# Kernel optimization log

Hardware: AMD Instinct MI355X
Metric: run time of the kernel (lower is better)

Reference implementation:

```python
import jax, jax.numpy as jnp
from jax import lax
import numpy as np

SEQ, BATCH, IN, H = 512, 256, 180, 8


def _lstm_layer(x, w_ih, w_hh, b_ih, b_hh):
    # x: [S, B, I]; PyTorch gate order: i, f, g, o stacked along 4H
    S, B, _ = x.shape
    Hh = w_hh.shape[1]
    # input contribution for all timesteps at once (one big GEMM)
    xg = jnp.einsum('sbi,gi->sbg', x, w_ih) + b_ih + b_hh  # [S, B, 4H]

    def step(carry, xt):
        h, c = carry
        g = xt + h @ w_hh.T  # [B, 4H]
        i, f, gg, o = jnp.split(g, 4, axis=-1)
        i = jax.nn.sigmoid(i)
        f = jax.nn.sigmoid(f)
        gg = jnp.tanh(gg)
        o = jax.nn.sigmoid(o)
        c = f * c + i * gg
        h = o * jnp.tanh(c)
        return (h, c), h

    init = (jnp.zeros((B, Hh), x.dtype), jnp.zeros((B, Hh), x.dtype))
    _, ys = lax.scan(step, init, xg)
    return ys  # [S, B, H]


def setup_inputs() -> dict:
    key = jax.random.key(0)
    ks = jax.random.split(key, 11)
    s = 1.0 / np.sqrt(H)  # PyTorch LSTM init scale
    return {
        'x': jax.random.normal(ks[0], (SEQ, BATCH, IN), jnp.float32),
        'w_ih0': jax.random.uniform(ks[1], (4 * H, IN), jnp.float32, -s, s),
        'w_hh0': jax.random.uniform(ks[2], (4 * H, H), jnp.float32, -s, s),
        'b_ih0': jax.random.uniform(ks[3], (4 * H,), jnp.float32, -s, s),
        'b_hh0': jax.random.uniform(ks[4], (4 * H,), jnp.float32, -s, s),
        'w_ih1': jax.random.uniform(ks[5], (4 * H, H), jnp.float32, -s, s),
        'w_hh1': jax.random.uniform(ks[6], (4 * H, H), jnp.float32, -s, s),
        'b_ih1': jax.random.uniform(ks[7], (4 * H,), jnp.float32, -s, s),
        'b_hh1': jax.random.uniform(ks[8], (4 * H,), jnp.float32, -s, s),
        'w_reg': jax.random.uniform(ks[9], (2, H), jnp.float32, -s, s),
        'b_reg': jax.random.uniform(ks[10], (2,), jnp.float32, -s, s),
    }


def reference(x, w_ih0, w_hh0, b_ih0, b_hh0, w_ih1, w_hh1, b_ih1, b_hh1, w_reg, b_reg):
    h1 = _lstm_layer(x, w_ih0, w_hh0, b_ih0, b_hh0)   # [S, B, H]
    h2 = _lstm_layer(h1, w_ih1, w_hh1, b_ih1, b_hh1)  # [S, B, H]
    S, B, Hh = h2.shape
    flat = h2.reshape(S * B, Hh)
    return flat @ w_reg.T + b_reg  # [S*B, 2]
```

## Files before the change

kernel.cpp:

```cpp
#include <hip/hip_runtime.h>

#define S_  512
#define B_  256
#define NIN 180

typedef float v2 __attribute__((ext_vector_type(2)));

#define SSIG  -1.4426950408889634f
#define STANH -2.8853900817779268f

#define QP_X1 0xB1
#define QP_X2 0x4E
#define QP_X3 0x1B
#define ROR4  0x124
#define ROR8  0x128

template<int CTRL>
__device__ __forceinline__ float dppf(float x) {
    return __uint_as_float((unsigned)__builtin_amdgcn_update_dpp(
        0, (int)__float_as_uint(x), CTRL, 0xF, 0xF, true));
}

#define ROTS8(h, r) do { \
    r[0] = (h); \
    r[1] = dppf<QP_X1>(h); \
    r[2] = dppf<QP_X2>(h); \
    r[3] = dppf<QP_X3>(h); \
    r[4] = dppf<ROR4>(h); \
    r[5] = dppf<QP_X1>(r[4]); \
    r[6] = dppf<QP_X2>(r[4]); \
    r[7] = dppf<QP_X3>(r[4]); \
} while (0)

__global__ __launch_bounds__(256) void xg_gemm(
    const float* __restrict__ x, const float* __restrict__ w,
    const float* __restrict__ bi, const float* __restrict__ bh,
    float* __restrict__ xg2)
{
    __shared__ float wt[NIN][32];
    __shared__ float bias[32];
    const int tid = threadIdx.x;
    for (int idx = tid; idx < NIN * 32; idx += 256) {
        int g = idx / NIN, i = idx - g * NIN;
        float sc = ((g >> 3) == 2) ? STANH : SSIG;
        wt[i][g] = sc * w[idx];
    }
    if (tid < 32) {
        float sc = ((tid >> 3) == 2) ? STANH : SSIG;
        bias[tid] = sc * (bi[tid] + bh[tid]);
    }
    __syncthreads();

    const int rg = tid >> 3;
    const int gq = tid & 7;
    const int s  = blockIdx.x >> 1;
    const int b0 = (blockIdx.x & 1) * 128 + rg * 4;
    const float* xr = x + ((size_t)s * B_ + b0) * NIN;

    float4 acc[4];
    #pragma unroll
    for (int r = 0; r < 4; ++r) acc[r] = float4{0.f, 0.f, 0.f, 0.f};

    float4 rv[2][4];
    #pragma unroll
    for (int r = 0; r < 4; ++r) {
        rv[0][r] = *(const float4*)(xr + (size_t)r * NIN + 0);
        rv[1][r] = *(const float4*)(xr + (size_t)r * NIN + 4);
    }

    #pragma unroll
    for (int ii = 0; ii < 45; ++ii) {
        const int sl = ii & 1;
        float4 xa[4];
        #pragma unroll
        for (int r = 0; r < 4; ++r) xa[r] = rv[sl][r];
        if (ii < 43) {
            #pragma unroll
            for (int r = 0; r < 4; ++r)
                rv[sl][r] = *(const float4*)(xr + (size_t)r * NIN + 4 * (ii + 2));
        }
        #pragma unroll
        for (int e = 0; e < 4; ++e) {
            float4 wv = *(const float4*)&wt[4 * ii + e][gq * 4];
            #pragma unroll
            for (int r = 0; r < 4; ++r) {
                float xe = (e == 0) ? xa[r].x : (e == 1) ? xa[r].y
                         : (e == 2) ? xa[r].z : xa[r].w;
                acc[r].x = __builtin_fmaf(xe, wv.x, acc[r].x);
                acc[r].y = __builtin_fmaf(xe, wv.y, acc[r].y);
                acc[r].z = __builtin_fmaf(xe, wv.z, acc[r].z);
                acc[r].w = __builtin_fmaf(xe, wv.w, acc[r].w);
            }
        }
    }

    float4 bv = *(const float4*)&bias[gq * 4];
    const int g0 = 4 * gq, q = g0 >> 3, j0 = g0 & 7, cls = q >> 1, qb = q & 1;
    #pragma unroll
    for (int r = 0; r < 4; ++r) {
        int b = b0 + r;
        size_t base = (((size_t)s * 64 + (b >> 2)) * 64
                      + (b & 3) * 16 + qb * 8 + j0) * 2 + cls;
        xg2[base + 0] = acc[r].x + bv.x;
        xg2[base + 2] = acc[r].y + bv.y;
        xg2[base + 4] = acc[r].z + bv.z;
        xg2[base + 6] = acc[r].w + bv.w;
    }
}

__global__ __launch_bounds__(128, 1) void lstm_scan(
    const float* __restrict__ xg,
    const float* __restrict__ w_hh0,
    const float* __restrict__ w_ih1, const float* __restrict__ w_hh1,
    const float* __restrict__ b_ih1, const float* __restrict__ b_hh1,
    const float* __restrict__ w_reg, const float* __restrict__ b_reg,
    float* __restrict__ out)
{
    __shared__ float a1buf[2][128];

    const int lt = threadIdx.x & 63;
    const int j  = lt & 7;
    const int b3 = (lt >> 3) & 1;
    const int cc = lt >> 4;
    const bool b3z = (b3 == 0);
    const int bid = blockIdx.x;

    const int gA = b3 * 8 + j;
    const int gB = (2 + b3) * 8 + j;
    const float sB_ = b3z ? STANH : SSIG;
    const float aB  = b3z ? 2.0f : 1.0f;
    const float bB  = b3z ? -1.0f : 0.0f;

    auto COMBINE2 = [&](float tA, float tB, float& c, float& h) {
        float m  = tA * tB;
        float mr = dppf<ROR8>(m);
        float fa = dppf<ROR8>(tA);
        float ob = dppf<ROR8>(tB);
        float ig = b3z ? m  : mr;
        float f  = b3z ? fa : tA;
        float o  = b3z ? ob : tB;
        c = __builtin_fmaf(f, c, ig);
        float th = __builtin_fmaf(2.0f, __builtin_amdgcn_rcpf(
            1.0f + __builtin_amdgcn_exp2f(STANH * c)), -1.0f);
        h = o * th;
    };

    if (threadIdx.x < 64) {
        v2 w0p[8], wi1p[8];
        #pragma unroll
        for (int m = 0; m < 8; ++m) {
            int k = j ^ m;
            w0p[m]  = v2{SSIG * w_hh0[gA * 8 + k], sB_ * w_hh0[gB * 8 + k]};
            wi1p[m] = v2{SSIG * w_ih1[gA * 8 + k], sB_ * w_ih1[gB * 8 + k]};
        }
        const v2 b1p = v2{SSIG * (b_ih1[gA] + b_hh1[gA]),
                          sB_  * (b_ih1[gB] + b_hh1[gB])};

        float h0p = 0.f, c0v = 0.f;
        const float* xrow = xg + (size_t)bid * 128;
        v2 xq[8];
        #pragma unroll
        for (int k2 = 0; k2 < 8; ++k2) {
            xq[k2] = *(const v2*)(xrow + lt * 2);
            xrow += 8192;
        }

        auto ASTEP = [&](v2& xr, int slot, bool pref) {
            v2 xc = xr;
            if (pref) { xr = *(const v2*)(xrow + lt * 2); xrow += 8192; }
            float r0[8];
            ROTS8(h0p, r0);
            v2 a0 = xc, a1p = b1p;
            #pragma unroll
            for (int m = 0; m < 8; ++m) {
                v2 rm = v2{r0[m], r0[m]};
                a0  = __builtin_elementwise_fma(w0p[m], rm, a0);
                a1p = __builtin_elementwise_fma(wi1p[m], rm, a1p);
            }
            *(v2*)&a1buf[slot][lt * 2] = a1p;
            float eA = __builtin_amdgcn_exp2f(a0.x);
            float eB = __builtin_amdgcn_exp2f(a0.y);
            float tA = __builtin_amdgcn_rcpf(1.0f + eA);
            float tB = __builtin_fmaf(aB, __builtin_amdgcn_rcpf(1.0f + eB), bB);
            COMBINE2(tA, tB, c0v, h0p);
            __syncthreads();
        };

        #pragma unroll
        for (int k2 = 0; k2 < 8; ++k2) ASTEP(xq[k2], k2 & 1, true);
        for (int tb = 8; tb < 504; tb += 8) {
            #pragma unroll
            for (int k2 = 0; k2 < 8; ++k2) ASTEP(xq[k2], k2 & 1, true);
        }
        #pragma unroll
        for (int k2 = 0; k2 < 8; ++k2) ASTEP(xq[k2], k2 & 1, false);

        {
            float r0[8];
            ROTS8(h0p, r0);
            v2 a1p = b1p;
            #pragma unroll
            for (int m = 0; m < 8; ++m) {
                v2 rm = v2{r0[m], r0[m]};
                a1p = __builtin_elementwise_fma(wi1p[m], rm, a1p);
            }
            *(v2*)&a1buf[0][lt * 2] = a1p;
            __syncthreads();
        }
    } else {
        v2 wh1p[8];
        float wrl[8];
        #pragma unroll
        for (int m = 0; m < 8; ++m) {
            int k = j ^ m;
            wh1p[m] = v2{SSIG * w_hh1[gA * 8 + k], sB_ * w_hh1[gB * 8 + k]};
            wrl[m]  = w_reg[b3 * 8 + k];
        }
        const float br  = b_reg[b3];
        const bool isl  = (j == 0);
        const int  ooff = (bid * 4 + cc) * 2 + b3;

        float h1p = 0.f, c1v = 0.f;

        auto BSTEP = [&](int slot, bool dostore, int yrow) {
            v2 a1 = *(const v2*)&a1buf[slot][lt * 2];
            float r1[8];
            ROTS8(h1p, r1);
            #pragma unroll
            for (int m = 0; m < 8; ++m) {
                v2 rm = v2{r1[m], r1[m]};
                a1 = __builtin_elementwise_fma(wh1p[m], rm, a1);
            }
            float p = br;
            #pragma unroll
            for (int m = 0; m < 8; ++m) p = __builtin_fmaf(wrl[m], r1[m], p);
            float eA = __builtin_amdgcn_exp2f(a1.x);
            float eB = __builtin_amdgcn_exp2f(a1.y);
            float tA = __builtin_amdgcn_rcpf(1.0f + eA);
            float tB = __builtin_fmaf(aB, __builtin_amdgcn_rcpf(1.0f + eB), bB);
            if (dostore && isl) out[(size_t)yrow * 512 + ooff] = p;
            COMBINE2(tA, tB, c1v, h1p);
        };

        __syncthreads();
        __syncthreads();
        for (int u = 2; u < 512; ++u) {
            BSTEP((u - 1) & 1, u >= 3, u - 3);
            __syncthreads();
        }
        BSTEP(1, true, 509);
        __syncthreads();
        BSTEP(0, true, 510);
        {
            float r1[8];
            ROTS8(h1p, r1);
            float p = br;
            #pragma unroll
            for (int m = 0; m < 8; ++m) p = __builtin_fmaf(wrl[m], r1[m], p);
            if (isl) out[(size_t)511 * 512 + ooff] = p;
        }
    }
}

extern "C" void kernel_launch(void* const* d_in, const int* in_sizes, int n_in,
                              void* d_out, int out_size, void* d_ws, size_t ws_size,
                              hipStream_t stream) {
    (void)in_sizes; (void)n_in; (void)out_size; (void)ws_size;
    const float* x     = (const float*)d_in[0];
    const float* w_ih0 = (const float*)d_in[1];
    const float* w_hh0 = (const float*)d_in[2];
    const float* b_ih0 = (const float*)d_in[3];
    const float* b_hh0 = (const float*)d_in[4];
    const float* w_ih1 = (const float*)d_in[5];
    const float* w_hh1 = (const float*)d_in[6];
    const float* b_ih1 = (const float*)d_in[7];
    const float* b_hh1 = (const float*)d_in[8];
    const float* w_reg = (const float*)d_in[9];
    const float* b_reg = (const float*)d_in[10];
    float* out = (float*)d_out;
    float* xg2 = (float*)d_ws;

    xg_gemm<<<1024, 256, 0, stream>>>(x, w_ih0, b_ih0, b_hh0, xg2);
    lstm_scan<<<64, 128, 0, stream>>>(xg2, w_hh0, w_ih1, w_hh1, b_ih1, b_hh1,
                                      w_reg, b_reg, out);
}
```

Measured before the change: 136.3 us.

## Batch layer handoff through 16-slot ring and retile xg GEMM to 8 rows per thread

The scan kernel's layer-0 wave now writes layer-1 input contributions into a 16-slot shared ring and synchronises once every four timesteps instead of every step. The layer-1 wave consumes the ring with matching barriers and runs the output projection only when it is needed. The input GEMM is retiled so each thread computes 8 batch rows with packed v2 FMAs and a 3-deep prefetch, using a permuted weight column order so it can write float4 stores. The fewer barriers should shorten the serial scan, at the cost of more shared memory, more registers and more complex indexing.

```diff
diff --git a/kernel.cpp b/kernel.cpp
--- a/kernel.cpp
+++ b/kernel.cpp
@@ -41,70 +41,84 @@
     __shared__ float bias[32];
     const int tid = threadIdx.x;
     for (int idx = tid; idx < NIN * 32; idx += 256) {
-        int g = idx / NIN, i = idx - g * NIN;
+        int c = idx / NIN, i = idx - c * NIN;
+        int t = c >> 2, e = c & 3;
+        int g = (t >> 2) * 8 + (t & 3) * 2 + (e >> 1) + ((e & 1) << 4);
         float sc = ((g >> 3) == 2) ? STANH : SSIG;
-        wt[i][g] = sc * w[idx];
+        wt[i][c] = sc * w[g * NIN + i];
     }
     if (tid < 32) {
-        float sc = ((tid >> 3) == 2) ? STANH : SSIG;
-        bias[tid] = sc * (bi[tid] + bh[tid]);
+        int c = tid, t = c >> 2, e = c & 3;
+        int g = (t >> 2) * 8 + (t & 3) * 2 + (e >> 1) + ((e & 1) << 4);
+        float sc = ((g >> 3) == 2) ? STANH : SSIG;
+        bias[c] = sc * (bi[g] + bh[g]);
     }
     __syncthreads();
 
     const int rg = tid >> 3;
-    const int gq = tid & 7;
-    const int s  = blockIdx.x >> 1;
-    const int b0 = (blockIdx.x & 1) * 128 + rg * 4;
+    const int t8 = tid & 7;
+    const int s  = blockIdx.x;
+    const int b0 = rg * 8;
     const float* xr = x + ((size_t)s * B_ + b0) * NIN;
 
-    float4 acc[4];
+    v2 acc[8][2];
     #pragma unroll
-    for (int r = 0; r < 4; ++r) acc[r] = float4{0.f, 0.f, 0.f, 0.f};
-
-    float4 rv[2][4];
+    for (int r = 0; r < 8; ++r) { acc[r][0] = v2{0.f, 0.f}; acc[r][1] = v2{0.f, 0.f}; }
+
+    float4 xb[3][8];
     #pragma unroll
-    for (int r = 0; r < 4; ++r) {
-        rv[0][r] = *(const float4*)(xr + (size_t)r * NIN + 0);
-        rv[1][r] = *(const float4*)(xr + (size_t)r * NIN + 4);
-    }
-
+    for (int d = 0; d < 3; ++d)
+        #pragma unroll
+        for (int r = 0; r < 8; ++r)
+            xb[d][r] = *(const float4*)(xr + (size_t)r * NIN + 4 * d);
+
+    auto GSTEP = [&](int ii, int d, bool pref) {
+        float4 xn[8];
+        if (pref) {
+            #pragma unroll
+            for (int r = 0; r < 8; ++r)
+                xn[r] = *(const float4*)(xr + (size_t)r * NIN + 4 * (ii + 3));
+        }
+        #pragma unroll
+        for (int e = 0; e < 4; ++e) {
+            float4 wv = *(const float4*)&wt[4 * ii + e][t8 * 4];
+            v2 wlo = v2{wv.x, wv.y}, whi = v2{wv.z, wv.w};
+            #pragma unroll
+            for (int r = 0; r < 8; ++r) {
+                float xe = (e == 0) ? xb[d][r].x : (e == 1) ? xb[d][r].y
+                         : (e == 2) ? xb[d][r].z : xb[d][r].w;
+                v2 xv = v2{xe, xe};
+                acc[r][0] = __builtin_elementwise_fma(wlo, xv, acc[r][0]);
+                acc[r][1] = __builtin_elementwise_fma(whi, xv, acc[r][1]);
+            }
+        }
+        if (pref) {
+            #pragma unroll
+            for (int r = 0; r < 8; ++r) xb[d][r] = xn[r];
+        }
+    };
+
+    for (int r = 0; r < 14; ++r) {
+        GSTEP(3 * r + 0, 0, true);
+        GSTEP(3 * r + 1, 1, true);
+        GSTEP(3 * r + 2, 2, true);
+    }
+    GSTEP(42, 0, false);
+    GSTEP(43, 1, false);
+    GSTEP(44, 2, false);
+
+    float4 bv = *(const float4*)&bias[t8 * 4];
+    const int toff = (t8 >> 2) * 16 + (t8 & 3) * 4;
     #pragma unroll
-    for (int ii = 0; ii < 45; ++ii) {
-        const int sl = ii & 1;
-        float4 xa[4];
-        #pragma unroll
-        for (int r = 0; r < 4; ++r) xa[r] = rv[sl][r];
-        if (ii < 43) {
-            #pragma unroll
-            for (int r = 0; r < 4; ++r)
-                rv[sl][r] = *(const float4*)(xr + (size_t)r * NIN + 4 * (ii + 2));
-        }
-        #pragma unroll
-        for (int e = 0; e < 4; ++e) {
-            float4 wv = *(const float4*)&wt[4 * ii + e][gq * 4];
-            #pragma unroll
-            for (int r = 0; r < 4; ++r) {
-                float xe = (e == 0) ? xa[r].x : (e == 1) ? xa[r].y
-                         : (e == 2) ? xa[r].z : xa[r].w;
-                acc[r].x = __builtin_fmaf(xe, wv.x, acc[r].x);
-                acc[r].y = __builtin_fmaf(xe, wv.y, acc[r].y);
-                acc[r].z = __builtin_fmaf(xe, wv.z, acc[r].z);
-                acc[r].w = __builtin_fmaf(xe, wv.w, acc[r].w);
-            }
-        }
-    }
-
-    float4 bv = *(const float4*)&bias[gq * 4];
-    const int g0 = 4 * gq, q = g0 >> 3, j0 = g0 & 7, cls = q >> 1, qb = q & 1;
-    #pragma unroll
-    for (int r = 0; r < 4; ++r) {
+    for (int r = 0; r < 8; ++r) {
         int b = b0 + r;
-        size_t base = (((size_t)s * 64 + (b >> 2)) * 64
-                      + (b & 3) * 16 + qb * 8 + j0) * 2 + cls;
-        xg2[base + 0] = acc[r].x + bv.x;
-        xg2[base + 2] = acc[r].y + bv.y;
-        xg2[base + 4] = acc[r].z + bv.z;
-        xg2[base + 6] = acc[r].w + bv.w;
+        float4 o;
+        o.x = acc[r][0].x + bv.x;
+        o.y = acc[r][0].y + bv.y;
+        o.z = acc[r][1].x + bv.z;
+        o.w = acc[r][1].y + bv.w;
+        size_t base = ((size_t)s * 64 + (b >> 2)) * 128 + (b & 3) * 32 + toff;
+        *(float4*)(xg2 + base) = o;
     }
 }
 
@@ -116,7 +130,7 @@
     const float* __restrict__ w_reg, const float* __restrict__ b_reg,
     float* __restrict__ out)
 {
-    __shared__ float a1buf[2][128];
+    __shared__ float abuf[16][128];
 
     const int lt = threadIdx.x & 63;
     const int j  = lt & 7;
@@ -165,7 +179,7 @@
             xrow += 8192;
         }
 
-        auto ASTEP = [&](v2& xr, int slot, bool pref) {
+        auto ASTEP = [&](v2& xr, int slot, bool store, bool pref) {
             v2 xc = xr;
             if (pref) { xr = *(const v2*)(xrow + lt * 2); xrow += 8192; }
             float r0[8];
@@ -177,24 +191,36 @@
                 a0  = __builtin_elementwise_fma(w0p[m], rm, a0);
                 a1p = __builtin_elementwise_fma(wi1p[m], rm, a1p);
             }
-            *(v2*)&a1buf[slot][lt * 2] = a1p;
+            if (store) *(v2*)&abuf[slot][lt * 2] = a1p;
             float eA = __builtin_amdgcn_exp2f(a0.x);
             float eB = __builtin_amdgcn_exp2f(a0.y);
             float tA = __builtin_amdgcn_rcpf(1.0f + eA);
             float tB = __builtin_fmaf(aB, __builtin_amdgcn_rcpf(1.0f + eB), bB);
             COMBINE2(tA, tB, c0v, h0p);
-            __syncthreads();
         };
 
-        #pragma unroll
-        for (int k2 = 0; k2 < 8; ++k2) ASTEP(xq[k2], k2 & 1, true);
-        for (int tb = 8; tb < 504; tb += 8) {
-            #pragma unroll
-            for (int k2 = 0; k2 < 8; ++k2) ASTEP(xq[k2], k2 & 1, true);
-        }
-        #pragma unroll
-        for (int k2 = 0; k2 < 8; ++k2) ASTEP(xq[k2], k2 & 1, false);
-
+        ASTEP(xq[0], 0, false, true);
+        ASTEP(xq[1], 0, true, true);
+        ASTEP(xq[2], 1, true, true);
+        ASTEP(xq[3], 2, true, true);
+        __syncthreads();
+        ASTEP(xq[4], 3, true, true);
+        ASTEP(xq[5], 4, true, true);
+        ASTEP(xq[6], 5, true, true);
+        ASTEP(xq[7], 6, true, true);
+        __syncthreads();
+        for (int m = 0; m < 31; ++m) {
+            #pragma unroll
+            for (int k = 0; k < 16; ++k) {
+                ASTEP(xq[k & 7], (7 + k) & 15, true, true);
+                if ((k & 3) == 3) __syncthreads();
+            }
+        }
+        #pragma unroll
+        for (int k = 0; k < 8; ++k) {
+            ASTEP(xq[k], (7 + k) & 15, true, false);
+            if ((k & 3) == 3) __syncthreads();
+        }
         {
             float r0[8];
             ROTS8(h0p, r0);
@@ -204,7 +230,7 @@
                 v2 rm = v2{r0[m], r0[m]};
                 a1p = __builtin_elementwise_fma(wi1p[m], rm, a1p);
             }
-            *(v2*)&a1buf[0][lt * 2] = a1p;
+            *(v2*)&abuf[15][lt * 2] = a1p;
             __syncthreads();
         }
     } else {
@@ -218,12 +244,12 @@
         }
         const float br  = b_reg[b3];
         const bool isl  = (j == 0);
-        const int  ooff = (bid * 4 + cc) * 2 + b3;
+        float* op = out + (size_t)(bid * 4 + cc) * 2 + b3;
 
         float h1p = 0.f, c1v = 0.f;
 
-        auto BSTEP = [&](int slot, bool dostore, int yrow) {
-            v2 a1 = *(const v2*)&a1buf[slot][lt * 2];
+        auto BSTEP = [&](int slot, bool doproj) {
+            v2 a1 = *(const v2*)&abuf[slot][lt * 2];
             float r1[8];
             ROTS8(h1p, r1);
             #pragma unroll
@@ -231,33 +257,49 @@
                 v2 rm = v2{r1[m], r1[m]};
                 a1 = __builtin_elementwise_fma(wh1p[m], rm, a1);
             }
-            float p = br;
-            #pragma unroll
-            for (int m = 0; m < 8; ++m) p = __builtin_fmaf(wrl[m], r1[m], p);
             float eA = __builtin_amdgcn_exp2f(a1.x);
             float eB = __builtin_amdgcn_exp2f(a1.y);
             float tA = __builtin_amdgcn_rcpf(1.0f + eA);
             float tB = __builtin_fmaf(aB, __builtin_amdgcn_rcpf(1.0f + eB), bB);
-            if (dostore && isl) out[(size_t)yrow * 512 + ooff] = p;
+            if (doproj) {
+                float p = br;
+                #pragma unroll
+                for (int m = 0; m < 8; ++m) p = __builtin_fmaf(wrl[m], r1[m], p);
+                if (isl) *op = p;
+                op += 512;
+            }
             COMBINE2(tA, tB, c1v, h1p);
         };
 
         __syncthreads();
         __syncthreads();
-        for (int u = 2; u < 512; ++u) {
-            BSTEP((u - 1) & 1, u >= 3, u - 3);
-            __syncthreads();
-        }
-        BSTEP(1, true, 509);
-        __syncthreads();
-        BSTEP(0, true, 510);
+        #pragma unroll
+        for (int k = 0; k < 16; ++k) {
+            BSTEP(k, k != 0);
+            if ((k & 3) == 3) __syncthreads();
+        }
+        for (int m = 1; m < 31; ++m) {
+            #pragma unroll
+            for (int k = 0; k < 16; ++k) {
+                BSTEP(k, true);
+                if ((k & 3) == 3) __syncthreads();
+            }
+        }
+        #pragma unroll
+        for (int k = 0; k < 8; ++k) {
+            BSTEP(k, true);
+            if ((k & 3) == 3) __syncthreads();
+        }
+        __syncthreads();
+        #pragma unroll
+        for (int k = 8; k < 16; ++k) BSTEP(k, true);
         {
             float r1[8];
             ROTS8(h1p, r1);
             float p = br;
             #pragma unroll
             for (int m = 0; m < 8; ++m) p = __builtin_fmaf(wrl[m], r1[m], p);
-            if (isl) out[(size_t)511 * 512 + ooff] = p;
+            if (isl) *op = p;
         }
     }
 }
@@ -280,7 +322,7 @@
     float* out = (float*)d_out;
     float* xg2 = (float*)d_ws;
 
-    xg_gemm<<<1024, 256, 0, stream>>>(x, w_ih0, b_ih0, b_hh0, xg2);
+    xg_gemm<<<512, 256, 0, stream>>>(x, w_ih0, b_ih0, b_hh0, xg2);
     lstm_scan<<<64, 128, 0, stream>>>(xg2, w_hh0, w_ih1, w_hh1, b_ih1, b_hh1,
                                       w_reg, b_reg, out);
 }
```

Result: faster. 129.6 us (-4.9%).
